# Optimization experiments

Measured on AMD Instinct MI355X. Metric: run time of the kernel, lower is better.

Reference implementation:

```python
import jax, jax.numpy as jnp
import numpy as np

N_NODES = 50000
N_EDGES = 800000
NUM_HEADS = 4
HEAD_DIM = 32
IN_DIM = 128
NEG_SLOPE = 0.2


def setup_inputs() -> dict:
    key = jax.random.key(0)
    k1, k2, k3, k4, k5, k6 = jax.random.split(key, 6)
    x = jax.random.normal(k1, (N_NODES, IN_DIM), dtype=jnp.float32)
    W = jax.random.normal(k2, (NUM_HEADS * HEAD_DIM, IN_DIM), dtype=jnp.float32) * 0.05
    attn_l = jax.random.normal(k3, (NUM_HEADS, HEAD_DIM), dtype=jnp.float32) * 0.05
    attn_r = jax.random.normal(k4, (NUM_HEADS, HEAD_DIM), dtype=jnp.float32) * 0.05
    src = jax.random.randint(k5, (N_EDGES,), 0, N_NODES, dtype=jnp.int32)
    dst = jnp.sort(jax.random.randint(k6, (N_EDGES,), 0, N_NODES, dtype=jnp.int32))
    return {"x": x, "W": W, "attn_l": attn_l, "attn_r": attn_r, "src": src, "dst": dst}


def reference(x, W, attn_l, attn_r, src, dst):
    N = x.shape[0]
    H, D = attn_l.shape
    # linear projection: [N, H*D] -> [N, H, D]
    feat = (x @ W.T).reshape(N, H, D)
    # per-node attention terms  [N, H]
    el = jnp.einsum('nhd,hd->nh', feat, attn_l)
    er = jnp.einsum('nhd,hd->nh', feat, attn_r)
    # per-edge logits (u_add_v) + leaky relu  [E, H]
    e = el[src] + er[dst]
    e = jnp.where(e > 0, e, NEG_SLOPE * e)
    # edge softmax segmented by destination node
    e_max = jax.ops.segment_max(e, dst, num_segments=N)          # [N, H]
    e_exp = jnp.exp(e - e_max[dst])                              # [E, H]
    denom = jax.ops.segment_sum(e_exp, dst, num_segments=N)     # [N, H]
    alpha = e_exp / denom[dst]                                   # [E, H]
    # attention-weighted neighbor aggregation  [N, H, D]
    out = jax.ops.segment_sum(alpha[:, :, None] * feat[src], dst, num_segments=N)
    return out.reshape(N, H * D)
```

## Files before the change

### kernel.cpp

```cpp
#include <hip/hip_runtime.h>
#include <math.h>

#define NN 50000
#define NE 800000
#define NH 4
#define HD 32
#define FD 128
#define NTILE 3125

typedef __attribute__((ext_vector_type(8))) short short8;
typedef __attribute__((ext_vector_type(4))) float floatx4;

__device__ __forceinline__ unsigned short f2bf(float f) {
    union { float f; unsigned u; } v; v.f = f;
    unsigned u = v.u;
    return (unsigned short)((u + 0x7FFFu + ((u >> 16) & 1u)) >> 16);
}
__device__ __forceinline__ float bf_lo(unsigned u) {
    union { unsigned u; float f; } v; v.u = u << 16; return v.f;
}
__device__ __forceinline__ float bf_hi(unsigned u) {
    union { unsigned u; float f; } v; v.u = u & 0xFFFF0000u; return v.f;
}

__global__ __launch_bounds__(512) void k_gemm_fused(const float* __restrict__ x,
                                                    const float* __restrict__ W,
                                                    const float* __restrict__ al,
                                                    const float* __restrict__ ar,
                                                    unsigned short* __restrict__ feat_bf,
                                                    float* __restrict__ el,
                                                    float* __restrict__ er) {
    __shared__ unsigned short Wl[FD * 136];
    const int tid = threadIdx.x;

    for (int p = tid; p < FD * 64; p += 512) {
        int c = p >> 6, k2 = (p & 63) * 2;
        float2 wv = *(const float2*)&W[c * FD + k2];
        *(unsigned*)&Wl[c * 136 + k2] =
            (unsigned)f2bf(wv.x) | ((unsigned)f2bf(wv.y) << 16);
    }
    __syncthreads();

    const int wv_id = tid >> 6, lane = tid & 63;
    const int col = lane & 15, quad = lane >> 4;

    float alr[8], arr[8];
    #pragma unroll
    for (int ct = 0; ct < 8; ++ct) {
        alr[ct] = al[col + 16 * ct];
        arr[ct] = ar[col + 16 * ct];
    }

    for (int tile = blockIdx.x * 8 + wv_id; tile < NTILE; tile += gridDim.x * 8) {
        const int n0 = tile * 16;

        short8 afrag[4];
        const float* xrow = x + (size_t)(n0 + col) * FD;
        #pragma unroll
        for (int s = 0; s < 4; ++s) {
            float4 u0 = *(const float4*)&xrow[s * 32 + quad * 8];
            float4 u1 = *(const float4*)&xrow[s * 32 + quad * 8 + 4];
            short8 a;
            a[0] = (short)f2bf(u0.x); a[1] = (short)f2bf(u0.y);
            a[2] = (short)f2bf(u0.z); a[3] = (short)f2bf(u0.w);
            a[4] = (short)f2bf(u1.x); a[5] = (short)f2bf(u1.y);
            a[6] = (short)f2bf(u1.z); a[7] = (short)f2bf(u1.w);
            afrag[s] = a;
        }

        floatx4 acc[8];
        #pragma unroll
        for (int ct = 0; ct < 8; ++ct) acc[ct] = (floatx4){0.f, 0.f, 0.f, 0.f};

        #pragma unroll
        for (int ct = 0; ct < 8; ++ct) {
            #pragma unroll
            for (int s = 0; s < 4; ++s) {
                short8 b = *(const short8*)&Wl[(ct * 16 + col) * 136 + s * 32 + quad * 8];
                acc[ct] = __builtin_amdgcn_mfma_f32_16x16x32_bf16(afrag[s], b, acc[ct], 0, 0, 0);
            }
        }

        #pragma unroll
        for (int ct = 0; ct < 8; ++ct) {
            #pragma unroll
            for (int r = 0; r < 4; ++r) {
                feat_bf[(size_t)(n0 + quad * 4 + r) * FD + ct * 16 + col] = f2bf(acc[ct][r]);
            }
        }

        #pragma unroll
        for (int r = 0; r < 4; ++r) {
            float ev[8];
            #pragma unroll
            for (int hh = 0; hh < NH; ++hh) {
                ev[hh]     = acc[2 * hh][r] * alr[2 * hh] + acc[2 * hh + 1][r] * alr[2 * hh + 1];
                ev[4 + hh] = acc[2 * hh][r] * arr[2 * hh] + acc[2 * hh + 1][r] * arr[2 * hh + 1];
            }
            #pragma unroll
            for (int m = 1; m < 16; m <<= 1) {
                #pragma unroll
                for (int j = 0; j < 8; ++j) ev[j] += __shfl_xor(ev[j], m);
            }
            if (col == 0) {
                int n = n0 + quad * 4 + r;
                *(float4*)&el[n * NH] = make_float4(ev[0], ev[1], ev[2], ev[3]);
                *(float4*)&er[n * NH] = make_float4(ev[4], ev[5], ev[6], ev[7]);
            }
        }
    }
}

__global__ void k_edgew(const float* __restrict__ el,
                        const float* __restrict__ er,
                        const int* __restrict__ src,
                        const int* __restrict__ dst,
                        float* __restrict__ wE,
                        int* __restrict__ rows) {
    int e = blockIdx.x * blockDim.x + threadIdx.x;
    if (e >= NE) return;
    int sj = src[e], dj = dst[e];

    if (e == 0) {
        for (int n = 0; n <= dj; ++n) rows[n] = 0;
    } else {
        int prev = dst[e - 1];
        for (int n = prev + 1; n <= dj; ++n) rows[n] = e;
    }
    if (e == NE - 1) {
        for (int n = dj + 1; n <= NN; ++n) rows[n] = NE;
    }

    float4 el4 = *(const float4*)&el[sj * NH];
    float4 er4 = *(const float4*)&er[dj * NH];
    float4 w;
    float lg, z;
    lg = el4.x + er4.x; z = fmaxf(lg, 0.2f * lg); w.x = __expf(z);
    lg = el4.y + er4.y; z = fmaxf(lg, 0.2f * lg); w.y = __expf(z);
    lg = el4.z + er4.z; z = fmaxf(lg, 0.2f * lg); w.z = __expf(z);
    lg = el4.w + er4.w; z = fmaxf(lg, 0.2f * lg); w.w = __expf(z);
    *(float4*)&wE[e * NH] = w;
}

__global__ __launch_bounds__(256) void k_aggregate(const unsigned short* __restrict__ feat_bf,
                                                   const float* __restrict__ wE,
                                                   const int* __restrict__ src,
                                                   const int* __restrict__ rows,
                                                   float* __restrict__ out) {
    const int wave = threadIdx.x >> 6;
    const int lane = threadIdx.x & 63;
    const int n = blockIdx.x * 4 + wave;
    if (n >= NN) return;

    const int s = rows[n], t = rows[n + 1];
    const int q  = lane >> 4;
    const int lp = lane & 15;
    const int h  = lp >> 2;
    const int dimoff = 8 * lp;

    float acc[8] = {0.f, 0.f, 0.f, 0.f, 0.f, 0.f, 0.f, 0.f};
    float den = 0.f;

    for (int e = s; e < t; e += 16) {
        int   sjv[4];
        float wv4[4];
        #pragma unroll
        for (int u = 0; u < 4; ++u) {
            int ei = e + 4 * u + q;
            int ec = (ei < t) ? ei : (t - 1);
            sjv[u] = src[ec];
            wv4[u] = (ei < t) ? wE[ec * NH + h] : 0.f;
        }
        uint4 uvv[4];
        #pragma unroll
        for (int u = 0; u < 4; ++u)
            uvv[u] = *(const uint4*)&feat_bf[(size_t)sjv[u] * FD + dimoff];
        #pragma unroll
        for (int u = 0; u < 4; ++u) {
            float w = wv4[u];
            uint4 uv = uvv[u];
            acc[0] += w * bf_lo(uv.x); acc[1] += w * bf_hi(uv.x);
            acc[2] += w * bf_lo(uv.y); acc[3] += w * bf_hi(uv.y);
            acc[4] += w * bf_lo(uv.z); acc[5] += w * bf_hi(uv.z);
            acc[6] += w * bf_lo(uv.w); acc[7] += w * bf_hi(uv.w);
            den += w;
        }
    }

    #pragma unroll
    for (int m = 16; m < 64; m <<= 1) {
        #pragma unroll
        for (int j = 0; j < 8; ++j) acc[j] += __shfl_xor(acc[j], m);
        den += __shfl_xor(den, m);
    }

    if (q == 0) {
        const float rden = (den > 0.f) ? 1.f / den : 0.f;
        float* op = out + (size_t)n * FD + dimoff;
        *(float4*)op       = make_float4(acc[0] * rden, acc[1] * rden, acc[2] * rden, acc[3] * rden);
        *(float4*)(op + 4) = make_float4(acc[4] * rden, acc[5] * rden, acc[6] * rden, acc[7] * rden);
    }
}

extern "C" void kernel_launch(void* const* d_in, const int* in_sizes, int n_in,
                              void* d_out, int out_size, void* d_ws, size_t ws_size,
                              hipStream_t stream) {
    const float* x  = (const float*)d_in[0];
    const float* W  = (const float*)d_in[1];
    const float* al = (const float*)d_in[2];
    const float* ar = (const float*)d_in[3];
    const int* src  = (const int*)d_in[4];
    const int* dst  = (const int*)d_in[5];
    float* out = (float*)d_out;

    unsigned short* feat_bf = (unsigned short*)d_ws;
    float* el = (float*)(feat_bf + (size_t)NN * FD);
    float* er = el + (size_t)NN * NH;
    int*   rows = (int*)(er + (size_t)NN * NH);
    float* wE = (float*)(((uintptr_t)(rows + NN + 1) + 15) & ~(uintptr_t)15);

    k_gemm_fused<<<256, 512, 0, stream>>>(x, W, al, ar, feat_bf, el, er);
    k_edgew<<<(NE + 255) / 256, 256, 0, stream>>>(el, er, src, dst, wE, rows);
    k_aggregate<<<(NN + 3) / 4, 256, 0, stream>>>(feat_bf, wE, src, rows, out);
}
```

Before: 133.6 us.

## Fold attention vectors into projection via extra MFMA, add nontemporal memory ops

Adds a small prep kernel that folds attn_l/attn_r into W, producing a 16x128 bf16 matrix. The GEMM then computes el/er with one extra MFMA tile instead of per-row dot products and shuffle reductions. The grid grows from 256 to 392 blocks, and the edge and aggregate kernels use nontemporal loads and stores for src, dst, wE and out. This removes shuffle-reduction work but adds a kernel launch, and the bf16 rounding of the folded matrix changes numerics slightly. Splitting the vector output stores into scalar nontemporal stores may weaken coalescing.

```diff
diff --git a/kernel.cpp b/kernel.cpp
--- a/kernel.cpp
+++ b/kernel.cpp
@@ -23,14 +23,32 @@
     union { unsigned u; float f; } v; v.u = u & 0xFFFF0000u; return v.f;
 }
 
-__global__ __launch_bounds__(512) void k_gemm_fused(const float* __restrict__ x,
-                                                    const float* __restrict__ W,
-                                                    const float* __restrict__ al,
-                                                    const float* __restrict__ ar,
-                                                    unsigned short* __restrict__ feat_bf,
-                                                    float* __restrict__ el,
-                                                    float* __restrict__ er) {
+__global__ void k_prep(const float* __restrict__ W,
+                       const float* __restrict__ al,
+                       const float* __restrict__ ar,
+                       unsigned short* __restrict__ Gbf) {
+    int p = blockIdx.x * blockDim.x + threadIdx.x;
+    if (p >= 16 * 128) return;
+    int j = p >> 7, k = p & 127;
+    float g = 0.f;
+    if (j < 8) {
+        int hh = j & 3;
+        const float* av = (j < 4) ? al : ar;
+        #pragma unroll
+        for (int d = 0; d < 32; ++d)
+            g += av[hh * 32 + d] * W[(size_t)(hh * 32 + d) * FD + k];
+    }
+    Gbf[p] = f2bf(g);
+}
+
+__global__ __launch_bounds__(512) void k_gemm(const float* __restrict__ x,
+                                              const float* __restrict__ W,
+                                              const unsigned short* __restrict__ Gbf,
+                                              unsigned short* __restrict__ feat_bf,
+                                              float* __restrict__ el,
+                                              float* __restrict__ er) {
     __shared__ unsigned short Wl[FD * 136];
+    __shared__ unsigned short ABl[16 * 136];
     const int tid = threadIdx.x;
 
     for (int p = tid; p < FD * 64; p += 512) {
@@ -39,17 +57,14 @@
         *(unsigned*)&Wl[c * 136 + k2] =
             (unsigned)f2bf(wv.x) | ((unsigned)f2bf(wv.y) << 16);
     }
+    for (int p = tid; p < 16 * 128; p += 512) {
+        int j = p >> 7, k = p & 127;
+        ABl[j * 136 + k] = Gbf[p];
+    }
     __syncthreads();
 
     const int wv_id = tid >> 6, lane = tid & 63;
     const int col = lane & 15, quad = lane >> 4;
-
-    float alr[8], arr[8];
-    #pragma unroll
-    for (int ct = 0; ct < 8; ++ct) {
-        alr[ct] = al[col + 16 * ct];
-        arr[ct] = ar[col + 16 * ct];
-    }
 
     for (int tile = blockIdx.x * 8 + wv_id; tile < NTILE; tile += gridDim.x * 8) {
         const int n0 = tile * 16;
@@ -69,6 +84,7 @@
         }
 
         floatx4 acc[8];
+        floatx4 accE = (floatx4){0.f, 0.f, 0.f, 0.f};
         #pragma unroll
         for (int ct = 0; ct < 8; ++ct) acc[ct] = (floatx4){0.f, 0.f, 0.f, 0.f};
 
@@ -80,6 +96,11 @@
                 acc[ct] = __builtin_amdgcn_mfma_f32_16x16x32_bf16(afrag[s], b, acc[ct], 0, 0, 0);
             }
         }
+        #pragma unroll
+        for (int s = 0; s < 4; ++s) {
+            short8 b = *(const short8*)&ABl[col * 136 + s * 32 + quad * 8];
+            accE = __builtin_amdgcn_mfma_f32_16x16x32_bf16(afrag[s], b, accE, 0, 0, 0);
+        }
 
         #pragma unroll
         for (int ct = 0; ct < 8; ++ct) {
@@ -88,25 +109,12 @@
                 feat_bf[(size_t)(n0 + quad * 4 + r) * FD + ct * 16 + col] = f2bf(acc[ct][r]);
             }
         }
-
-        #pragma unroll
-        for (int r = 0; r < 4; ++r) {
-            float ev[8];
+        if (col < 8) {
+            float* base = (col < 4) ? el : er;
+            int hh = col & 3;
             #pragma unroll
-            for (int hh = 0; hh < NH; ++hh) {
-                ev[hh]     = acc[2 * hh][r] * alr[2 * hh] + acc[2 * hh + 1][r] * alr[2 * hh + 1];
-                ev[4 + hh] = acc[2 * hh][r] * arr[2 * hh] + acc[2 * hh + 1][r] * arr[2 * hh + 1];
-            }
-            #pragma unroll
-            for (int m = 1; m < 16; m <<= 1) {
-                #pragma unroll
-                for (int j = 0; j < 8; ++j) ev[j] += __shfl_xor(ev[j], m);
-            }
-            if (col == 0) {
-                int n = n0 + quad * 4 + r;
-                *(float4*)&el[n * NH] = make_float4(ev[0], ev[1], ev[2], ev[3]);
-                *(float4*)&er[n * NH] = make_float4(ev[4], ev[5], ev[6], ev[7]);
-            }
+            for (int r = 0; r < 4; ++r)
+                base[(n0 + quad * 4 + r) * NH + hh] = accE[r];
         }
     }
 }
@@ -119,12 +127,13 @@
                         int* __restrict__ rows) {
     int e = blockIdx.x * blockDim.x + threadIdx.x;
     if (e >= NE) return;
-    int sj = src[e], dj = dst[e];
+    int sj = __builtin_nontemporal_load(&src[e]);
+    int dj = __builtin_nontemporal_load(&dst[e]);
 
     if (e == 0) {
         for (int n = 0; n <= dj; ++n) rows[n] = 0;
     } else {
-        int prev = dst[e - 1];
+        int prev = __builtin_nontemporal_load(&dst[e - 1]);
         for (int n = prev + 1; n <= dj; ++n) rows[n] = e;
     }
     if (e == NE - 1) {
@@ -133,13 +142,17 @@
 
     float4 el4 = *(const float4*)&el[sj * NH];
     float4 er4 = *(const float4*)&er[dj * NH];
-    float4 w;
     float lg, z;
-    lg = el4.x + er4.x; z = fmaxf(lg, 0.2f * lg); w.x = __expf(z);
-    lg = el4.y + er4.y; z = fmaxf(lg, 0.2f * lg); w.y = __expf(z);
-    lg = el4.z + er4.z; z = fmaxf(lg, 0.2f * lg); w.z = __expf(z);
-    lg = el4.w + er4.w; z = fmaxf(lg, 0.2f * lg); w.w = __expf(z);
-    *(float4*)&wE[e * NH] = w;
+    float w0, w1, w2, w3;
+    lg = el4.x + er4.x; z = fmaxf(lg, 0.2f * lg); w0 = __expf(z);
+    lg = el4.y + er4.y; z = fmaxf(lg, 0.2f * lg); w1 = __expf(z);
+    lg = el4.z + er4.z; z = fmaxf(lg, 0.2f * lg); w2 = __expf(z);
+    lg = el4.w + er4.w; z = fmaxf(lg, 0.2f * lg); w3 = __expf(z);
+    float* wp = &wE[e * NH];
+    __builtin_nontemporal_store(w0, wp + 0);
+    __builtin_nontemporal_store(w1, wp + 1);
+    __builtin_nontemporal_store(w2, wp + 2);
+    __builtin_nontemporal_store(w3, wp + 3);
 }
 
 __global__ __launch_bounds__(256) void k_aggregate(const unsigned short* __restrict__ feat_bf,
@@ -168,8 +181,8 @@
         for (int u = 0; u < 4; ++u) {
             int ei = e + 4 * u + q;
             int ec = (ei < t) ? ei : (t - 1);
-            sjv[u] = src[ec];
-            wv4[u] = (ei < t) ? wE[ec * NH + h] : 0.f;
+            sjv[u] = __builtin_nontemporal_load(&src[ec]);
+            wv4[u] = (ei < t) ? __builtin_nontemporal_load(&wE[ec * NH + h]) : 0.f;
         }
         uint4 uvv[4];
         #pragma unroll
@@ -197,8 +210,9 @@
     if (q == 0) {
         const float rden = (den > 0.f) ? 1.f / den : 0.f;
         float* op = out + (size_t)n * FD + dimoff;
-        *(float4*)op       = make_float4(acc[0] * rden, acc[1] * rden, acc[2] * rden, acc[3] * rden);
-        *(float4*)(op + 4) = make_float4(acc[4] * rden, acc[5] * rden, acc[6] * rden, acc[7] * rden);
+        #pragma unroll
+        for (int j = 0; j < 8; ++j)
+            __builtin_nontemporal_store(acc[j] * rden, op + j);
     }
 }
 
@@ -218,8 +232,10 @@
     float* er = el + (size_t)NN * NH;
     int*   rows = (int*)(er + (size_t)NN * NH);
     float* wE = (float*)(((uintptr_t)(rows + NN + 1) + 15) & ~(uintptr_t)15);
-
-    k_gemm_fused<<<256, 512, 0, stream>>>(x, W, al, ar, feat_bf, el, er);
+    unsigned short* Gbf = (unsigned short*)(wE + (size_t)NE * NH);
+
+    k_prep<<<8, 256, 0, stream>>>(W, al, ar, Gbf);
+    k_gemm<<<392, 512, 0, stream>>>(x, W, Gbf, feat_bf, el, er);
     k_edgew<<<(NE + 255) / 256, 256, 0, stream>>>(el, er, src, dst, wE, rows);
     k_aggregate<<<(NN + 3) / 4, 256, 0, stream>>>(feat_bf, wE, src, rows, out);
 }
```

Measured after the change: 139.0 us. 4.1% more time.
